# Kernel tuning notes

Hardware: AMD Instinct MI355X
Metric: run time of the kernel (lower is better)

## Reference

```python
import jax, jax.numpy as jnp
import numpy as np

B, T, C = 4, 4096, 1024
H, CS = 16, 128
D = C // H
EPS = 1e-5

def _ln(x, g, b):
    m = jnp.mean(x, axis=-1, keepdims=True)
    v = jnp.var(x, axis=-1, keepdims=True)
    return (x - m) * jax.lax.rsqrt(v + EPS) * g + b

def setup_inputs() -> dict:
    key = jax.random.key(0)
    ks = jax.random.split(key, 12)
    s_c = 1.0 / np.sqrt(C)
    s_2d = 1.0 / np.sqrt(2 * D)
    return {
        "x": jax.random.normal(ks[0], (B, T, C), jnp.float32),
        "mark_W": jax.random.normal(ks[1], (C, C), jnp.float32) * s_c,
        "mark_b": jnp.zeros((C,), jnp.float32),
        "gate_W": jax.random.normal(ks[2], (C, C), jnp.float32) * s_c,
        "gate_b": jnp.zeros((C,), jnp.float32),
        "carry_g": jnp.ones((D,), jnp.float32),
        "carry_b": jnp.zeros((D,), jnp.float32),
        "card_g": jnp.ones((D,), jnp.float32),
        "card_b": jnp.zeros((D,), jnp.float32),
        "ho1_W": jax.random.normal(ks[3], (2 * D, 2 * D), jnp.float32) * s_2d,
        "ho1_b": jnp.zeros((2 * D,), jnp.float32),
        "ho2_W": jax.random.normal(ks[4], (2 * D, D), jnp.float32) * s_2d,
        "ho2_b": jnp.zeros((D,), jnp.float32),
        "proj_W": jax.random.normal(ks[5], (C, C), jnp.float32) * s_c * 0.02,
        "proj_b": jnp.zeros((C,), jnp.float32),
        "ln_g": jnp.ones((C,), jnp.float32),
        "ln_b": jnp.zeros((C,), jnp.float32),
    }

def reference(x, mark_W, mark_b, gate_W, gate_b, carry_g, carry_b,
              card_g, card_b, ho1_W, ho1_b, ho2_W, ho2_b,
              proj_W, proj_b, ln_g, ln_b):
    b, t, c = x.shape
    nc = t // CS  # T chosen divisible by chunk_size -> pad_len = 0
    pm = x @ mark_W + mark_b                       # [B,T,C]
    gates = jax.nn.sigmoid(x @ gate_W + gate_b)    # [B,T,C]

    def chunks(a):  # [B,T,C] -> [B,H,nc,CS,D]
        return a.reshape(b, nc, CS, H, D).transpose(0, 3, 1, 2, 4)

    x_h = chunks(x)
    gm = chunks(gates) * chunks(pm)                # gated marks
    lcm = jnp.cumsum(gm, axis=3)                   # local prefix sum within chunk
    chunk_sums = lcm[:, :, :, -1, :]               # [B,H,nc,D]
    carry_cum = jnp.cumsum(chunk_sums, axis=2)
    carries = jnp.concatenate(
        [jnp.zeros((b, H, 1, D), x.dtype), carry_cum[:, :, :-1, :]], axis=2)
    nrm_carry = _ln(carries, carry_g, carry_b)[:, :, :, None, :]  # [B,H,nc,1,D]
    mwc = lcm + nrm_carry                          # marks with carry
    cards_local = jnp.concatenate([nrm_carry, mwc[:, :, :, :-1, :]], axis=3)
    cards = _ln(cards_local, card_g, card_b)
    comb = jnp.concatenate([x_h, cards], axis=-1)  # [B,H,nc,CS,2D]
    h = jax.nn.gelu(comb @ ho1_W + ho1_b, approximate=False)
    ho = h @ ho2_W + ho2_b                         # [B,H,nc,CS,D]
    out = ho.transpose(0, 2, 3, 1, 4).reshape(b, t, c)
    out = out @ proj_W + proj_b
    out = _ln(out, ln_g, ln_b)
    return x + out
```

## Files before the change

kernel.cpp:

```cpp
#include <hip/hip_runtime.h>
#include <hip/hip_bf16.h>

typedef __bf16 bf16_t;
typedef __attribute__((ext_vector_type(8))) __bf16 bf16x8;
typedef __attribute__((ext_vector_type(4))) __bf16 bf16x4;
typedef __attribute__((ext_vector_type(4))) float f32x4;

static constexpr int Bn = 4, Tn = 4096, Cn = 1024, Hn = 16, CSn = 128, Dn = 64, NCn = 32;

#define DEVINL __device__ __forceinline__

DEVINL float wsum64(float v) {
  v += __shfl_xor(v, 32, 64);
  v += __shfl_xor(v, 16, 64);
  v += __shfl_xor(v, 8, 64);
  v += __shfl_xor(v, 4, 64);
  v += __shfl_xor(v, 2, 64);
  v += __shfl_xor(v, 1, 64);
  return v;
}

DEVINL float gelu_f(float v) {
  float x = v * 0.70710678f;
  float ax = fabsf(x);
  float t = 1.f / (1.f + 0.3275911f * ax);
  float poly = t * (0.254829592f +
               t * (-0.284496736f +
               t * (1.421413741f +
               t * (-1.453152027f +
               t * 1.061405429f))));
  float e = __expf(-ax * ax);
  float erfax = 1.f - poly * e;
  float erfx = copysignf(erfax, x);
  return 0.5f * v * (1.f + erfx);
}

DEVINL void gld16(const bf16_t* g, bf16_t* l) {
  __builtin_amdgcn_global_load_lds(
      (const __attribute__((address_space(1))) unsigned int*)(g),
      (__attribute__((address_space(3))) unsigned int*)(l), 16, 0, 0);
}

__global__ __launch_bounds__(256) void k_xbf(const float* __restrict__ in,
                                             bf16_t* __restrict__ out) {
  int i = blockIdx.x * 256 + threadIdx.x;
  float4 a = *reinterpret_cast<const float4*>(in + (size_t)i * 8);
  float4 b = *reinterpret_cast<const float4*>(in + (size_t)i * 8 + 4);
  bf16x8 o = {(bf16_t)a.x, (bf16_t)a.y, (bf16_t)a.z, (bf16_t)a.w,
              (bf16_t)b.x, (bf16_t)b.y, (bf16_t)b.z, (bf16_t)b.w};
  *reinterpret_cast<bf16x8*>(out + (size_t)i * 8) = o;
}

__global__ void k_transpose(const float* __restrict__ in, bf16_t* __restrict__ out,
                            int rows, int cols) {
  __shared__ float tile[64][65];
  int c0 = blockIdx.x * 64, r0 = blockIdx.y * 64;
  int tx = threadIdx.x & 63, ty = threadIdx.x >> 6;
#pragma unroll
  for (int i = ty; i < 64; i += 4)
    tile[i][tx] = in[(size_t)(r0 + i) * cols + c0 + tx];
  __syncthreads();
#pragma unroll
  for (int i = ty; i < 64; i += 4)
    out[(size_t)(c0 + i) * rows + r0 + tx] = (bf16_t)tile[tx][i];
}

__global__ __launch_bounds__(256, 3) void k_dualgemm_gm(
    const bf16_t* __restrict__ X, const bf16_t* __restrict__ Wtm,
    const bf16_t* __restrict__ Wtg, const float* __restrict__ bm,
    const float* __restrict__ bg, bf16_t* __restrict__ lcm,
    float* __restrict__ csum) {
  constexpr int K = Cn, N = Cn;
  constexpr int GP = 68;
  __shared__ __align__(16) bf16_t L[16384];
  __shared__ float tot[4][64];
  int tid = threadIdx.x;
  int Lb = blockIdx.x;
  int xcd = Lb & 7, jj = Lb >> 3;
  int nb = jj & 15, mb = xcd + 8 * (jj >> 4);
  int m0 = mb * 128, n0 = nb * 64;
  int wave = tid >> 6, lane = tid & 63;
  int wm = wave >> 1, wn = wave & 1;
  int lr = lane & 15, lk = lane >> 4;
  int rl = lane >> 2;
  int cl = (lane & 3) * 8;
  f32x4 accP[4][2] = {};
  f32x4 accG[4][2] = {};

  const bf16_t* Xb = X + (size_t)m0 * K;
  const bf16_t* Wmb = Wtm + (size_t)n0 * K;
  const bf16_t* Wgb = Wtg + (size_t)n0 * K;
  bf16_t* LA = L;
  bf16_t* LBm = L + 8192;
  bf16_t* LBg = L + 12288;

#define STAGE3(buf, kt)                                                    \
  {                                                                        \
    _Pragma("unroll")                                                      \
    for (int c = 0; c < 2; ++c) {                                          \
      int ch = wave * 2 + c;                                               \
      gld16(Xb + (size_t)(ch * 16 + rl) * K + (kt) * 32 + cl,              \
            LA + (buf) * 4096 + ch * 512);                                 \
    }                                                                      \
    size_t gob = (size_t)(wave * 16 + rl) * K + (kt) * 32 + cl;            \
    gld16(Wmb + gob, LBm + (buf) * 2048 + wave * 512);                     \
    gld16(Wgb + gob, LBg + (buf) * 2048 + wave * 512);                     \
  }

  STAGE3(0, 0);
  __syncthreads();
  int cur = 0;
  for (int kt = 0; kt < 32; ++kt) {
    if (kt < 31) STAGE3(cur ^ 1, kt + 1);
    bf16x8 af[4], bmf[2], bgf[2];
#pragma unroll
    for (int i = 0; i < 4; ++i)
      af[i] = *reinterpret_cast<const bf16x8*>(
          &LA[cur * 4096 + (wm * 64 + i * 16 + lr) * 32 + lk * 8]);
#pragma unroll
    for (int j = 0; j < 2; ++j) {
      bmf[j] = *reinterpret_cast<const bf16x8*>(
          &LBm[cur * 2048 + (wn * 32 + j * 16 + lr) * 32 + lk * 8]);
      bgf[j] = *reinterpret_cast<const bf16x8*>(
          &LBg[cur * 2048 + (wn * 32 + j * 16 + lr) * 32 + lk * 8]);
    }
#pragma unroll
    for (int i = 0; i < 4; ++i)
#pragma unroll
      for (int j = 0; j < 2; ++j) {
        accP[i][j] = __builtin_amdgcn_mfma_f32_16x16x32_bf16(af[i], bmf[j], accP[i][j], 0, 0, 0);
        accG[i][j] = __builtin_amdgcn_mfma_f32_16x16x32_bf16(af[i], bgf[j], accG[i][j], 0, 0, 0);
      }
    __syncthreads();
    cur ^= 1;
  }
#undef STAGE3

  bf16_t* G = L;
#pragma unroll
  for (int j = 0; j < 2; ++j) {
    int col = wn * 32 + j * 16 + lr;
    float bmv = bm[n0 + col], bgv = bg[n0 + col];
#pragma unroll
    for (int i = 0; i < 4; ++i) {
      int rbase = wm * 64 + i * 16 + lk * 4;
#pragma unroll
      for (int r = 0; r < 4; ++r) {
        float p = accP[i][j][r] + bmv;
        float g = accG[i][j][r] + bgv;
        float s = 1.f / (1.f + __expf(-g));
        G[(rbase + r) * GP + col] = (bf16_t)(s * p);
      }
    }
  }
  __syncthreads();
  {
    int col = tid & 63;
    int q = tid >> 6;
    float lsum = 0.f;
#pragma unroll 8
    for (int r = 0; r < 32; ++r)
      lsum += (float)G[(q * 32 + r) * GP + col];
    tot[q][col] = lsum;
    __syncthreads();
    float run = 0.f;
#pragma unroll
    for (int qq = 0; qq < 3; ++qq)
      if (qq < q) run += tot[qq][col];
    int gc = n0 + col;
    size_t obase = (size_t)(m0 + q * 32) * N + gc;
#pragma unroll 8
    for (int r = 0; r < 32; ++r) {
      run += (float)G[(q * 32 + r) * GP + col];
      lcm[obase + (size_t)r * N] = (bf16_t)run;
    }
    if (q == 3) {
      int bb = m0 >> 12;
      int ci = (m0 >> 7) & 31;
      csum[(((size_t)bb * Hn + (gc >> 6)) * NCn + ci) * 64 + (gc & 63)] = run;
    }
  }
}

__global__ __launch_bounds__(64) void k_carry_ln(const float* __restrict__ csum,
                                                 float* __restrict__ ncar,
                                                 const float* __restrict__ g,
                                                 const float* __restrict__ be) {
  int bh = blockIdx.x;
  int d = threadIdx.x;
  float gd = g[d], bd = be[d];
  float run = 0.f;
  for (int ci = 0; ci < NCn; ++ci) {
    float v = run;
    run += csum[((size_t)bh * NCn + ci) * 64 + d];
    float m = wsum64(v) * (1.f / 64.f);
    float dv = v - m;
    float var = wsum64(dv * dv) * (1.f / 64.f);
    ncar[((size_t)bh * NCn + ci) * 64 + d] = dv * rsqrtf(var + 1e-5f) * gd + bd;
  }
}

__global__ __launch_bounds__(256, 4) void k_ho_fused(
    const bf16_t* __restrict__ X, const bf16_t* __restrict__ lcm,
    const float* __restrict__ ncar, const float* __restrict__ cg,
    const float* __restrict__ cb, const bf16_t* __restrict__ W1t,
    const float* __restrict__ b1, const bf16_t* __restrict__ W2t,
    const float* __restrict__ b2, bf16_t* __restrict__ ho) {
  __shared__ __align__(16) bf16_t Cs[128][136];
  int tid = threadIdx.x;
  int ci = blockIdx.x & 31, bh = blockIdx.x >> 5;
  int h = bh & 15, b = bh >> 4;
  int wave = tid >> 6, lane = tid & 63;
  int wm = wave >> 1, wn = wave & 1;
  int lr = lane & 15, lk = lane >> 4;
  size_t xrow0 = (size_t)(b * Tn + ci * CSn);

  bf16x8 xf0[4], xf1[4];
#pragma unroll
  for (int i = 0; i < 4; ++i) {
    const bf16_t* xr = X + (xrow0 + wm * 64 + i * 16 + lr) * Cn + h * Dn + lk * 8;
    xf0[i] = *reinterpret_cast<const bf16x8*>(xr);
    xf1[i] = *reinterpret_cast<const bf16x8*>(xr + 32);
  }

  {
    int lg = lane >> 3;
    int le = lane & 7;
    int d0 = le * 8;
    const float* np = ncar + ((size_t)bh * NCn + ci) * 64 + d0;
    float ncv[8], ggv[8], bbv[8];
#pragma unroll
    for (int e = 0; e < 8; ++e) {
      ncv[e] = np[e];
      ggv[e] = cg[d0 + e];
      bbv[e] = cb[d0 + e];
    }
#pragma unroll
    for (int it = 0; it < 4; ++it) {
      int pr = wave * 32 + it * 8 + lg;
      float v[8];
      if (pr > 0) {
        bf16x8 lv = *reinterpret_cast<const bf16x8*>(
            lcm + (xrow0 + pr - 1) * Cn + h * Dn + d0);
#pragma unroll
        for (int e = 0; e < 8; ++e) v[e] = (float)lv[e] + ncv[e];
      } else {
#pragma unroll
        for (int e = 0; e < 8; ++e) v[e] = ncv[e];
      }
      float s = 0.f;
#pragma unroll
      for (int e = 0; e < 8; ++e) s += v[e];
      s += __shfl_xor(s, 1, 64);
      s += __shfl_xor(s, 2, 64);
      s += __shfl_xor(s, 4, 64);
      float mean = s * (1.f / 64.f);
      float q = 0.f;
#pragma unroll
      for (int e = 0; e < 8; ++e) { float dv = v[e] - mean; q += dv * dv; }
      q += __shfl_xor(q, 1, 64);
      q += __shfl_xor(q, 2, 64);
      q += __shfl_xor(q, 4, 64);
      float rs = rsqrtf(q * (1.f / 64.f) + 1e-5f);
      bf16x8 o;
#pragma unroll
      for (int e = 0; e < 8; ++e)
        o[e] = (bf16_t)((v[e] - mean) * rs * ggv[e] + bbv[e]);
      *reinterpret_cast<bf16x8*>(&Cs[pr][64 + d0]) = o;
    }
  }
  __syncthreads();
  f32x4 acc[4][4] = {};
#pragma unroll
  for (int ks = 0; ks < 4; ++ks) {
    bf16x8 af[4], bfr[4];
#pragma unroll
    for (int i = 0; i < 4; ++i) {
      if (ks == 0)      af[i] = xf0[i];
      else if (ks == 1) af[i] = xf1[i];
      else
        af[i] = *reinterpret_cast<const bf16x8*>(
            &Cs[wm * 64 + i * 16 + lr][64 + (ks - 2) * 32 + lk * 8]);
    }
#pragma unroll
    for (int j = 0; j < 4; ++j)
      bfr[j] = *reinterpret_cast<const bf16x8*>(
          W1t + (size_t)(wn * 64 + j * 16 + lr) * 128 + ks * 32 + lk * 8);
#pragma unroll
    for (int i = 0; i < 4; ++i)
#pragma unroll
      for (int j = 0; j < 4; ++j)
        acc[i][j] = __builtin_amdgcn_mfma_f32_16x16x32_bf16(af[i], bfr[j], acc[i][j], 0, 0, 0);
  }
  __syncthreads();
#pragma unroll
  for (int j = 0; j < 4; ++j) {
    int col = wn * 64 + j * 16 + lr;
    float bv = b1[col];
#pragma unroll
    for (int i = 0; i < 4; ++i) {
      int rbase = wm * 64 + i * 16 + lk * 4;
#pragma unroll
      for (int r = 0; r < 4; ++r)
        Cs[rbase + r][col] = (bf16_t)gelu_f(acc[i][j][r] + bv);
    }
  }
  __syncthreads();
  f32x4 acc2[2][4] = {};
#pragma unroll
  for (int ks = 0; ks < 4; ++ks) {
    bf16x8 af[2], bfr[4];
#pragma unroll
    for (int i = 0; i < 2; ++i)
      af[i] = *reinterpret_cast<const bf16x8*>(&Cs[wave * 32 + i * 16 + lr][ks * 32 + lk * 8]);
#pragma unroll
    for (int j = 0; j < 4; ++j)
      bfr[j] = *reinterpret_cast<const bf16x8*>(
          W2t + (size_t)(j * 16 + lr) * 128 + ks * 32 + lk * 8);
#pragma unroll
    for (int i = 0; i < 2; ++i)
#pragma unroll
      for (int j = 0; j < 4; ++j)
        acc2[i][j] = __builtin_amdgcn_mfma_f32_16x16x32_bf16(af[i], bfr[j], acc2[i][j], 0, 0, 0);
  }
#pragma unroll
  for (int j = 0; j < 4; ++j) {
    int dd = j * 16 + lr;
    float bv = b2[dd];
#pragma unroll
    for (int i = 0; i < 2; ++i) {
      int pbase = wave * 32 + i * 16 + lk * 4;
#pragma unroll
      for (int r = 0; r < 4; ++r)
        ho[(xrow0 + pbase + r) * Cn + h * Dn + dd] = (bf16_t)(acc2[i][j][r] + bv);
    }
  }
}

__global__ __launch_bounds__(256, 2) void k_gemm_bt(
    const bf16_t* __restrict__ A, const bf16_t* __restrict__ Wt,
    const float* __restrict__ bias, bf16_t* __restrict__ out) {
  constexpr int K = Cn, N = Cn;
  __shared__ __align__(16) bf16_t L[4][128 * 32];
  int tid = threadIdx.x;
  int Lb = blockIdx.x + 8 * blockIdx.y;
  int xcd = Lb & 7, jj = Lb >> 3;
  int nb = jj & 7, mb = xcd + 8 * (jj >> 3);
  int m0 = mb * 128, n0 = nb * 128;
  int wave = tid >> 6, lane = tid & 63;
  int wm = wave >> 1, wn = wave & 1;
  int lr = lane & 15, lk = lane >> 4;
  int rl = lane >> 2, cl = (lane & 3) * 8;
  f32x4 acc[4][4] = {};
  const bf16_t* Ab = A + (size_t)m0 * K;
  const bf16_t* Wb = Wt + (size_t)n0 * K;

#define STAGE2(buf, kt)                                                    \
  {                                                                        \
    _Pragma("unroll")                                                      \
    for (int c = 0; c < 2; ++c) {                                          \
      int ch = wave * 2 + c;                                               \
      size_t go = (size_t)(ch * 16 + rl) * K + (kt) * 32 + cl;             \
      int lo = ch * 512;                                                   \
      gld16(Ab + go, &L[0 + (buf)][lo]);                                   \
      gld16(Wb + go, &L[2 + (buf)][lo]);                                   \
    }                                                                      \
  }

  STAGE2(0, 0);
  __syncthreads();
  int cur = 0;
  for (int kt = 0; kt < 32; ++kt) {
    if (kt < 31) STAGE2(cur ^ 1, kt + 1);
    bf16x8 af[4], bfr[4];
#pragma unroll
    for (int i = 0; i < 4; ++i)
      af[i] = *reinterpret_cast<const bf16x8*>(&L[0 + cur][(wm * 64 + i * 16 + lr) * 32 + lk * 8]);
#pragma unroll
    for (int j = 0; j < 4; ++j)
      bfr[j] = *reinterpret_cast<const bf16x8*>(&L[2 + cur][(wn * 64 + j * 16 + lr) * 32 + lk * 8]);
#pragma unroll
    for (int i = 0; i < 4; ++i)
#pragma unroll
      for (int j = 0; j < 4; ++j)
        acc[i][j] = __builtin_amdgcn_mfma_f32_16x16x32_bf16(af[i], bfr[j], acc[i][j], 0, 0, 0);
    __syncthreads();
    cur ^= 1;
  }
#undef STAGE2
#pragma unroll
  for (int j = 0; j < 4; ++j) {
    int col = n0 + wn * 64 + j * 16 + lr;
    float bv = bias[col];
#pragma unroll
    for (int i = 0; i < 4; ++i) {
      int rbase = m0 + wm * 64 + i * 16 + lk * 4;
#pragma unroll
      for (int r = 0; r < 4; ++r)
        out[(size_t)(rbase + r) * N + col] = (bf16_t)(acc[i][j][r] + bv);
    }
  }
}

__global__ __launch_bounds__(256) void k_ln_residual(
    const bf16_t* __restrict__ pre, const float* __restrict__ X,
    const float* __restrict__ g, const float* __restrict__ be,
    float* __restrict__ out) {
  int row = blockIdx.x, t = threadIdx.x;
  size_t base = (size_t)row * Cn + t * 4;
  bf16x4 pv4 = *reinterpret_cast<const bf16x4*>(pre + base);
  float v0 = (float)pv4[0], v1 = (float)pv4[1], v2 = (float)pv4[2], v3 = (float)pv4[3];
  float s = v0 + v1 + v2 + v3;
  float q = v0 * v0 + v1 * v1 + v2 * v2 + v3 * v3;
  s = wsum64(s);
  q = wsum64(q);
  __shared__ float red[8];
  int wv = t >> 6, ln = t & 63;
  if (ln == 0) { red[wv] = s; red[4 + wv] = q; }
  __syncthreads();
  float tot = red[0] + red[1] + red[2] + red[3];
  float totq = red[4] + red[5] + red[6] + red[7];
  float mean = tot * (1.f / 1024.f);
  float var = totq * (1.f / 1024.f) - mean * mean;
  float rs = rsqrtf(fmaxf(var, 0.f) + 1e-5f);
  float4 xv = *reinterpret_cast<const float4*>(X + base);
  float4 gv = *reinterpret_cast<const float4*>(g + t * 4);
  float4 bv = *reinterpret_cast<const float4*>(be + t * 4);
  float4 o;
  o.x = (v0 - mean) * rs * gv.x + bv.x + xv.x;
  o.y = (v1 - mean) * rs * gv.y + bv.y + xv.y;
  o.z = (v2 - mean) * rs * gv.z + bv.z + xv.z;
  o.w = (v3 - mean) * rs * gv.w + bv.w + xv.w;
  *reinterpret_cast<float4*>(out + base) = o;
}

extern "C" void kernel_launch(void* const* d_in, const int* in_sizes, int n_in,
                              void* d_out, int out_size, void* d_ws, size_t ws_size,
                              hipStream_t stream) {
  const float* x       = (const float*)d_in[0];
  const float* mark_W  = (const float*)d_in[1];
  const float* mark_b  = (const float*)d_in[2];
  const float* gate_W  = (const float*)d_in[3];
  const float* gate_b  = (const float*)d_in[4];
  const float* carry_g = (const float*)d_in[5];
  const float* carry_b = (const float*)d_in[6];
  const float* card_g  = (const float*)d_in[7];
  const float* card_b  = (const float*)d_in[8];
  const float* ho1_W   = (const float*)d_in[9];
  const float* ho1_b   = (const float*)d_in[10];
  const float* ho2_W   = (const float*)d_in[11];
  const float* ho2_b   = (const float*)d_in[12];
  const float* proj_W  = (const float*)d_in[13];
  const float* proj_b  = (const float*)d_in[14];
  const float* ln_g    = (const float*)d_in[15];
  const float* ln_b    = (const float*)d_in[16];
  float* out = (float*)d_out;

  char* ws = (char*)d_ws;
  bf16_t* xbf    = (bf16_t*)(ws + 0);
  bf16_t* outpre = (bf16_t*)(ws + 0);
  bf16_t* gm     = (bf16_t*)(ws + 33554432);
  bf16_t* hobuf  = (bf16_t*)(ws + 100663296);
  float*  csum   = (float*)(ws + 134217728);
  float*  ncar   = (float*)(ws + 134742016);
  bf16_t* wtm    = (bf16_t*)(ws + 135266304);
  bf16_t* wtg    = (bf16_t*)(ws + 137363456);
  bf16_t* wtp    = (bf16_t*)(ws + 139460608);
  bf16_t* wt1    = (bf16_t*)(ws + 141557760);
  bf16_t* wt2    = (bf16_t*)(ws + 141590528);

  k_xbf<<<8192, 256, 0, stream>>>(x, xbf);
  k_transpose<<<dim3(16, 16), 256, 0, stream>>>(mark_W, wtm, 1024, 1024);
  k_transpose<<<dim3(16, 16), 256, 0, stream>>>(gate_W, wtg, 1024, 1024);
  k_transpose<<<dim3(16, 16), 256, 0, stream>>>(proj_W, wtp, 1024, 1024);
  k_transpose<<<dim3(2, 2),   256, 0, stream>>>(ho1_W, wt1, 128, 128);
  k_transpose<<<dim3(1, 2),   256, 0, stream>>>(ho2_W, wt2, 128, 64);

  k_dualgemm_gm<<<2048, 256, 0, stream>>>(xbf, wtm, wtg, mark_b, gate_b, gm, csum);
  k_carry_ln<<<64, 64, 0, stream>>>(csum, ncar, carry_g, carry_b);
  k_ho_fused<<<2048, 256, 0, stream>>>(xbf, gm, ncar, card_g, card_b,
                                       wt1, ho1_b, wt2, ho2_b, hobuf);
  k_gemm_bt<<<dim3(8, 128), 256, 0, stream>>>(hobuf, wtp, proj_b, outpre);
  k_ln_residual<<<16384, 256, 0, stream>>>(outpre, x, ln_g, ln_b, out);
}
```

Measured before the change: 264.7 us.

## Split ho_fused blocks into half chunks and read bf16 residual in LN

k_ho_fused now handles 64 rows per block instead of 128. That halves shared memory and the accumulator registers, doubles the grid to 4096 blocks, and raises the launch-bound occupancy target to 6. The final LN-residual kernel reads the residual x from the bf16 copy instead of fp32, which halves that read traffic. The output-pre buffer moves to its own workspace region so xbf is not overwritten. Adding the residual in bf16 instead of exact fp32 x costs some precision.

```diff
diff --git a/kernel.cpp b/kernel.cpp
--- a/kernel.cpp
+++ b/kernel.cpp
@@ -200,25 +200,28 @@
   }
 }
 
-__global__ __launch_bounds__(256, 4) void k_ho_fused(
+__global__ __launch_bounds__(256, 6) void k_ho_fused(
     const bf16_t* __restrict__ X, const bf16_t* __restrict__ lcm,
     const float* __restrict__ ncar, const float* __restrict__ cg,
     const float* __restrict__ cb, const bf16_t* __restrict__ W1t,
     const float* __restrict__ b1, const bf16_t* __restrict__ W2t,
     const float* __restrict__ b2, bf16_t* __restrict__ ho) {
-  __shared__ __align__(16) bf16_t Cs[128][136];
+  __shared__ __align__(16) bf16_t Cs[64][136];
   int tid = threadIdx.x;
-  int ci = blockIdx.x & 31, bh = blockIdx.x >> 5;
+  int idx = blockIdx.x;
+  int bh = idx >> 6;
+  int rem = idx & 63;
+  int ci = rem >> 1, half = rem & 1;
   int h = bh & 15, b = bh >> 4;
   int wave = tid >> 6, lane = tid & 63;
   int wm = wave >> 1, wn = wave & 1;
   int lr = lane & 15, lk = lane >> 4;
-  size_t xrow0 = (size_t)(b * Tn + ci * CSn);
-
-  bf16x8 xf0[4], xf1[4];
-#pragma unroll
-  for (int i = 0; i < 4; ++i) {
-    const bf16_t* xr = X + (xrow0 + wm * 64 + i * 16 + lr) * Cn + h * Dn + lk * 8;
+  size_t xrow0 = (size_t)(b * Tn + ci * CSn + half * 64);
+
+  bf16x8 xf0[2], xf1[2];
+#pragma unroll
+  for (int i = 0; i < 2; ++i) {
+    const bf16_t* xr = X + (xrow0 + wm * 32 + i * 16 + lr) * Cn + h * Dn + lk * 8;
     xf0[i] = *reinterpret_cast<const bf16x8*>(xr);
     xf1[i] = *reinterpret_cast<const bf16x8*>(xr + 32);
   }
@@ -236,10 +239,10 @@
       bbv[e] = cb[d0 + e];
     }
 #pragma unroll
-    for (int it = 0; it < 4; ++it) {
-      int pr = wave * 32 + it * 8 + lg;
+    for (int it = 0; it < 2; ++it) {
+      int pr = wave * 16 + it * 8 + lg;
       float v[8];
-      if (pr > 0) {
+      if (half || pr > 0) {
         bf16x8 lv = *reinterpret_cast<const bf16x8*>(
             lcm + (xrow0 + pr - 1) * Cn + h * Dn + d0);
 #pragma unroll
@@ -270,24 +273,24 @@
     }
   }
   __syncthreads();
-  f32x4 acc[4][4] = {};
+  f32x4 acc[2][4] = {};
 #pragma unroll
   for (int ks = 0; ks < 4; ++ks) {
-    bf16x8 af[4], bfr[4];
-#pragma unroll
-    for (int i = 0; i < 4; ++i) {
+    bf16x8 af[2], bfr[4];
+#pragma unroll
+    for (int i = 0; i < 2; ++i) {
       if (ks == 0)      af[i] = xf0[i];
       else if (ks == 1) af[i] = xf1[i];
       else
         af[i] = *reinterpret_cast<const bf16x8*>(
-            &Cs[wm * 64 + i * 16 + lr][64 + (ks - 2) * 32 + lk * 8]);
+            &Cs[wm * 32 + i * 16 + lr][64 + (ks - 2) * 32 + lk * 8]);
     }
 #pragma unroll
     for (int j = 0; j < 4; ++j)
       bfr[j] = *reinterpret_cast<const bf16x8*>(
           W1t + (size_t)(wn * 64 + j * 16 + lr) * 128 + ks * 32 + lk * 8);
 #pragma unroll
-    for (int i = 0; i < 4; ++i)
+    for (int i = 0; i < 2; ++i)
 #pragma unroll
       for (int j = 0; j < 4; ++j)
         acc[i][j] = __builtin_amdgcn_mfma_f32_16x16x32_bf16(af[i], bfr[j], acc[i][j], 0, 0, 0);
@@ -298,42 +301,35 @@
     int col = wn * 64 + j * 16 + lr;
     float bv = b1[col];
 #pragma unroll
-    for (int i = 0; i < 4; ++i) {
-      int rbase = wm * 64 + i * 16 + lk * 4;
+    for (int i = 0; i < 2; ++i) {
+      int rbase = wm * 32 + i * 16 + lk * 4;
 #pragma unroll
       for (int r = 0; r < 4; ++r)
         Cs[rbase + r][col] = (bf16_t)gelu_f(acc[i][j][r] + bv);
     }
   }
   __syncthreads();
-  f32x4 acc2[2][4] = {};
+  f32x4 acc2[4] = {};
 #pragma unroll
   for (int ks = 0; ks < 4; ++ks) {
-    bf16x8 af[2], bfr[4];
-#pragma unroll
-    for (int i = 0; i < 2; ++i)
-      af[i] = *reinterpret_cast<const bf16x8*>(&Cs[wave * 32 + i * 16 + lr][ks * 32 + lk * 8]);
+    bf16x8 af = *reinterpret_cast<const bf16x8*>(&Cs[wave * 16 + lr][ks * 32 + lk * 8]);
+    bf16x8 bfr[4];
 #pragma unroll
     for (int j = 0; j < 4; ++j)
       bfr[j] = *reinterpret_cast<const bf16x8*>(
           W2t + (size_t)(j * 16 + lr) * 128 + ks * 32 + lk * 8);
 #pragma unroll
-    for (int i = 0; i < 2; ++i)
-#pragma unroll
-      for (int j = 0; j < 4; ++j)
-        acc2[i][j] = __builtin_amdgcn_mfma_f32_16x16x32_bf16(af[i], bfr[j], acc2[i][j], 0, 0, 0);
+    for (int j = 0; j < 4; ++j)
+      acc2[j] = __builtin_amdgcn_mfma_f32_16x16x32_bf16(af, bfr[j], acc2[j], 0, 0, 0);
   }
 #pragma unroll
   for (int j = 0; j < 4; ++j) {
     int dd = j * 16 + lr;
     float bv = b2[dd];
-#pragma unroll
-    for (int i = 0; i < 2; ++i) {
-      int pbase = wave * 32 + i * 16 + lk * 4;
-#pragma unroll
-      for (int r = 0; r < 4; ++r)
-        ho[(xrow0 + pbase + r) * Cn + h * Dn + dd] = (bf16_t)(acc2[i][j][r] + bv);
-    }
+    int pbase = wave * 16 + lk * 4;
+#pragma unroll
+    for (int r = 0; r < 4; ++r)
+      ho[(xrow0 + pbase + r) * Cn + h * Dn + dd] = (bf16_t)(acc2[j][r] + bv);
   }
 }
 
@@ -403,7 +399,7 @@
 }
 
 __global__ __launch_bounds__(256) void k_ln_residual(
-    const bf16_t* __restrict__ pre, const float* __restrict__ X,
+    const bf16_t* __restrict__ pre, const bf16_t* __restrict__ Xb,
     const float* __restrict__ g, const float* __restrict__ be,
     float* __restrict__ out) {
   int row = blockIdx.x, t = threadIdx.x;
@@ -423,14 +419,14 @@
   float mean = tot * (1.f / 1024.f);
   float var = totq * (1.f / 1024.f) - mean * mean;
   float rs = rsqrtf(fmaxf(var, 0.f) + 1e-5f);
-  float4 xv = *reinterpret_cast<const float4*>(X + base);
+  bf16x4 xv4 = *reinterpret_cast<const bf16x4*>(Xb + base);
   float4 gv = *reinterpret_cast<const float4*>(g + t * 4);
   float4 bv = *reinterpret_cast<const float4*>(be + t * 4);
   float4 o;
-  o.x = (v0 - mean) * rs * gv.x + bv.x + xv.x;
-  o.y = (v1 - mean) * rs * gv.y + bv.y + xv.y;
-  o.z = (v2 - mean) * rs * gv.z + bv.z + xv.z;
-  o.w = (v3 - mean) * rs * gv.w + bv.w + xv.w;
+  o.x = (v0 - mean) * rs * gv.x + bv.x + (float)xv4[0];
+  o.y = (v1 - mean) * rs * gv.y + bv.y + (float)xv4[1];
+  o.z = (v2 - mean) * rs * gv.z + bv.z + (float)xv4[2];
+  o.w = (v3 - mean) * rs * gv.w + bv.w + (float)xv4[3];
   *reinterpret_cast<float4*>(out + base) = o;
 }
 
@@ -458,8 +454,8 @@
 
   char* ws = (char*)d_ws;
   bf16_t* xbf    = (bf16_t*)(ws + 0);
-  bf16_t* outpre = (bf16_t*)(ws + 0);
   bf16_t* gm     = (bf16_t*)(ws + 33554432);
+  bf16_t* outpre = (bf16_t*)(ws + 67108864);
   bf16_t* hobuf  = (bf16_t*)(ws + 100663296);
   float*  csum   = (float*)(ws + 134217728);
   float*  ncar   = (float*)(ws + 134742016);
@@ -478,8 +474,8 @@
 
   k_dualgemm_gm<<<2048, 256, 0, stream>>>(xbf, wtm, wtg, mark_b, gate_b, gm, csum);
   k_carry_ln<<<64, 64, 0, stream>>>(csum, ncar, carry_g, carry_b);
-  k_ho_fused<<<2048, 256, 0, stream>>>(xbf, gm, ncar, card_g, card_b,
+  k_ho_fused<<<4096, 256, 0, stream>>>(xbf, gm, ncar, card_g, card_b,
                                        wt1, ho1_b, wt2, ho2_b, hobuf);
   k_gemm_bt<<<dim3(8, 128), 256, 0, stream>>>(hobuf, wtp, proj_b, outpre);
-  k_ln_residual<<<16384, 256, 0, stream>>>(outpre, x, ln_g, ln_b, out);
-}
+  k_ln_residual<<<16384, 256, 0, stream>>>(outpre, xbf, ln_g, ln_b, out);
+}
```

New measurement: 290.1 us. 9.6% more time.

## Split card LayerNorm into its own kernel and read residual from bf16 copy

Applied to the files above, without the earlier changes.

Moves the per-chunk cards LayerNorm out of the fused head-output kernel into a separate kernel that writes a contiguous bf16 cards buffer. The fused kernel then loads that buffer into swizzled shared memory using direct global-to-LDS loads, which is meant to shorten its prologue. The final LayerNorm-residual kernel reads the residual from the bf16 copy of x instead of fp32 to halve that read traffic. This adds an extra launch and a global round trip for the cards buffer, and rounding the residual to bf16 loses precision in the output.

```diff
diff --git a/kernel.cpp b/kernel.cpp
--- a/kernel.cpp
+++ b/kernel.cpp
@@ -200,21 +200,85 @@
   }
 }
 
+__global__ __launch_bounds__(256) void k_cards(
+    const bf16_t* __restrict__ lcm, const float* __restrict__ ncar,
+    const float* __restrict__ cg, const float* __restrict__ cb,
+    bf16_t* __restrict__ cards) {
+  int blk = blockIdx.x;
+  int ci = blk & 31, bh = blk >> 5;
+  int h = bh & 15, b = bh >> 4;
+  int wave = threadIdx.x >> 6, lane = threadIdx.x & 63;
+  int lg = lane >> 3;
+  int le = lane & 7;
+  int d0 = le * 8;
+  size_t xrow0 = (size_t)(b * Tn + ci * CSn);
+  const float* np = ncar + ((size_t)bh * NCn + ci) * 64 + d0;
+  float ncv[8], ggv[8], bbv[8];
+#pragma unroll
+  for (int e = 0; e < 8; ++e) {
+    ncv[e] = np[e];
+    ggv[e] = cg[d0 + e];
+    bbv[e] = cb[d0 + e];
+  }
+#pragma unroll
+  for (int it = 0; it < 4; ++it) {
+    int pr = wave * 32 + it * 8 + lg;
+    float v[8];
+    if (pr > 0) {
+      bf16x8 lv = *reinterpret_cast<const bf16x8*>(
+          lcm + (xrow0 + pr - 1) * Cn + h * Dn + d0);
+#pragma unroll
+      for (int e = 0; e < 8; ++e) v[e] = (float)lv[e] + ncv[e];
+    } else {
+#pragma unroll
+      for (int e = 0; e < 8; ++e) v[e] = ncv[e];
+    }
+    float s = 0.f;
+#pragma unroll
+    for (int e = 0; e < 8; ++e) s += v[e];
+    s += __shfl_xor(s, 1, 64);
+    s += __shfl_xor(s, 2, 64);
+    s += __shfl_xor(s, 4, 64);
+    float mean = s * (1.f / 64.f);
+    float q = 0.f;
+#pragma unroll
+    for (int e = 0; e < 8; ++e) { float dv = v[e] - mean; q += dv * dv; }
+    q += __shfl_xor(q, 1, 64);
+    q += __shfl_xor(q, 2, 64);
+    q += __shfl_xor(q, 4, 64);
+    float rs = rsqrtf(q * (1.f / 64.f) + 1e-5f);
+    bf16x8 o;
+#pragma unroll
+    for (int e = 0; e < 8; ++e)
+      o[e] = (bf16_t)((v[e] - mean) * rs * ggv[e] + bbv[e]);
+    *reinterpret_cast<bf16x8*>(cards + ((size_t)blk * CSn + pr) * 64 + d0) = o;
+  }
+}
+
 __global__ __launch_bounds__(256, 4) void k_ho_fused(
-    const bf16_t* __restrict__ X, const bf16_t* __restrict__ lcm,
-    const float* __restrict__ ncar, const float* __restrict__ cg,
-    const float* __restrict__ cb, const bf16_t* __restrict__ W1t,
-    const float* __restrict__ b1, const bf16_t* __restrict__ W2t,
-    const float* __restrict__ b2, bf16_t* __restrict__ ho) {
-  __shared__ __align__(16) bf16_t Cs[128][136];
+    const bf16_t* __restrict__ X, const bf16_t* __restrict__ cards,
+    const bf16_t* __restrict__ W1t, const float* __restrict__ b1,
+    const bf16_t* __restrict__ W2t, const float* __restrict__ b2,
+    bf16_t* __restrict__ ho) {
+  __shared__ __align__(16) bf16_t S[128 * 136];
   int tid = threadIdx.x;
-  int ci = blockIdx.x & 31, bh = blockIdx.x >> 5;
+  int blk = blockIdx.x;
+  int ci = blk & 31, bh = blk >> 5;
   int h = bh & 15, b = bh >> 4;
   int wave = tid >> 6, lane = tid & 63;
   int wm = wave >> 1, wn = wave & 1;
   int lr = lane & 15, lk = lane >> 4;
   size_t xrow0 = (size_t)(b * Tn + ci * CSn);
 
+  {
+    const bf16_t* cbase = cards + (size_t)blk * CSn * 64;
+#pragma unroll
+    for (int c = 0; c < 4; ++c) {
+      int row = wave * 32 + c * 8 + (lane >> 3);
+      int c16 = (lane & 7) ^ (row & 7);
+      gld16(cbase + (size_t)row * 64 + c16 * 8, S + (wave * 32 + c * 8) * 64);
+    }
+  }
   bf16x8 xf0[4], xf1[4];
 #pragma unroll
   for (int i = 0; i < 4; ++i) {
@@ -222,54 +286,8 @@
     xf0[i] = *reinterpret_cast<const bf16x8*>(xr);
     xf1[i] = *reinterpret_cast<const bf16x8*>(xr + 32);
   }
-
-  {
-    int lg = lane >> 3;
-    int le = lane & 7;
-    int d0 = le * 8;
-    const float* np = ncar + ((size_t)bh * NCn + ci) * 64 + d0;
-    float ncv[8], ggv[8], bbv[8];
-#pragma unroll
-    for (int e = 0; e < 8; ++e) {
-      ncv[e] = np[e];
-      ggv[e] = cg[d0 + e];
-      bbv[e] = cb[d0 + e];
-    }
-#pragma unroll
-    for (int it = 0; it < 4; ++it) {
-      int pr = wave * 32 + it * 8 + lg;
-      float v[8];
-      if (pr > 0) {
-        bf16x8 lv = *reinterpret_cast<const bf16x8*>(
-            lcm + (xrow0 + pr - 1) * Cn + h * Dn + d0);
-#pragma unroll
-        for (int e = 0; e < 8; ++e) v[e] = (float)lv[e] + ncv[e];
-      } else {
-#pragma unroll
-        for (int e = 0; e < 8; ++e) v[e] = ncv[e];
-      }
-      float s = 0.f;
-#pragma unroll
-      for (int e = 0; e < 8; ++e) s += v[e];
-      s += __shfl_xor(s, 1, 64);
-      s += __shfl_xor(s, 2, 64);
-      s += __shfl_xor(s, 4, 64);
-      float mean = s * (1.f / 64.f);
-      float q = 0.f;
-#pragma unroll
-      for (int e = 0; e < 8; ++e) { float dv = v[e] - mean; q += dv * dv; }
-      q += __shfl_xor(q, 1, 64);
-      q += __shfl_xor(q, 2, 64);
-      q += __shfl_xor(q, 4, 64);
-      float rs = rsqrtf(q * (1.f / 64.f) + 1e-5f);
-      bf16x8 o;
-#pragma unroll
-      for (int e = 0; e < 8; ++e)
-        o[e] = (bf16_t)((v[e] - mean) * rs * ggv[e] + bbv[e]);
-      *reinterpret_cast<bf16x8*>(&Cs[pr][64 + d0]) = o;
-    }
-  }
-  __syncthreads();
+  __syncthreads();
+
   f32x4 acc[4][4] = {};
 #pragma unroll
   for (int ks = 0; ks < 4; ++ks) {
@@ -278,9 +296,11 @@
     for (int i = 0; i < 4; ++i) {
       if (ks == 0)      af[i] = xf0[i];
       else if (ks == 1) af[i] = xf1[i];
-      else
-        af[i] = *reinterpret_cast<const bf16x8*>(
-            &Cs[wm * 64 + i * 16 + lr][64 + (ks - 2) * 32 + lk * 8]);
+      else {
+        int row = wm * 64 + i * 16 + lr;
+        int c16 = ((ks - 2) * 4 + lk) ^ (lr & 7);
+        af[i] = *reinterpret_cast<const bf16x8*>(&S[row * 64 + c16 * 8]);
+      }
     }
 #pragma unroll
     for (int j = 0; j < 4; ++j)
@@ -302,7 +322,7 @@
       int rbase = wm * 64 + i * 16 + lk * 4;
 #pragma unroll
       for (int r = 0; r < 4; ++r)
-        Cs[rbase + r][col] = (bf16_t)gelu_f(acc[i][j][r] + bv);
+        S[(rbase + r) * 136 + col] = (bf16_t)gelu_f(acc[i][j][r] + bv);
     }
   }
   __syncthreads();
@@ -312,7 +332,8 @@
     bf16x8 af[2], bfr[4];
 #pragma unroll
     for (int i = 0; i < 2; ++i)
-      af[i] = *reinterpret_cast<const bf16x8*>(&Cs[wave * 32 + i * 16 + lr][ks * 32 + lk * 8]);
+      af[i] = *reinterpret_cast<const bf16x8*>(
+          &S[(wave * 32 + i * 16 + lr) * 136 + ks * 32 + lk * 8]);
 #pragma unroll
     for (int j = 0; j < 4; ++j)
       bfr[j] = *reinterpret_cast<const bf16x8*>(
@@ -403,7 +424,7 @@
 }
 
 __global__ __launch_bounds__(256) void k_ln_residual(
-    const bf16_t* __restrict__ pre, const float* __restrict__ X,
+    const bf16_t* __restrict__ pre, const bf16_t* __restrict__ Xb,
     const float* __restrict__ g, const float* __restrict__ be,
     float* __restrict__ out) {
   int row = blockIdx.x, t = threadIdx.x;
@@ -423,14 +444,14 @@
   float mean = tot * (1.f / 1024.f);
   float var = totq * (1.f / 1024.f) - mean * mean;
   float rs = rsqrtf(fmaxf(var, 0.f) + 1e-5f);
-  float4 xv = *reinterpret_cast<const float4*>(X + base);
+  bf16x4 xv4 = *reinterpret_cast<const bf16x4*>(Xb + base);
   float4 gv = *reinterpret_cast<const float4*>(g + t * 4);
   float4 bv = *reinterpret_cast<const float4*>(be + t * 4);
   float4 o;
-  o.x = (v0 - mean) * rs * gv.x + bv.x + xv.x;
-  o.y = (v1 - mean) * rs * gv.y + bv.y + xv.y;
-  o.z = (v2 - mean) * rs * gv.z + bv.z + xv.z;
-  o.w = (v3 - mean) * rs * gv.w + bv.w + xv.w;
+  o.x = (v0 - mean) * rs * gv.x + bv.x + (float)xv4[0];
+  o.y = (v1 - mean) * rs * gv.y + bv.y + (float)xv4[1];
+  o.z = (v2 - mean) * rs * gv.z + bv.z + (float)xv4[2];
+  o.w = (v3 - mean) * rs * gv.w + bv.w + (float)xv4[3];
   *reinterpret_cast<float4*>(out + base) = o;
 }
 
@@ -458,8 +479,9 @@
 
   char* ws = (char*)d_ws;
   bf16_t* xbf    = (bf16_t*)(ws + 0);
-  bf16_t* outpre = (bf16_t*)(ws + 0);
   bf16_t* gm     = (bf16_t*)(ws + 33554432);
+  bf16_t* cards  = (bf16_t*)(ws + 67108864);
+  bf16_t* outpre = (bf16_t*)(ws + 67108864);
   bf16_t* hobuf  = (bf16_t*)(ws + 100663296);
   float*  csum   = (float*)(ws + 134217728);
   float*  ncar   = (float*)(ws + 134742016);
@@ -478,8 +500,8 @@
 
   k_dualgemm_gm<<<2048, 256, 0, stream>>>(xbf, wtm, wtg, mark_b, gate_b, gm, csum);
   k_carry_ln<<<64, 64, 0, stream>>>(csum, ncar, carry_g, carry_b);
-  k_ho_fused<<<2048, 256, 0, stream>>>(xbf, gm, ncar, card_g, card_b,
-                                       wt1, ho1_b, wt2, ho2_b, hobuf);
+  k_cards<<<2048, 256, 0, stream>>>(gm, ncar, card_g, card_b, cards);
+  k_ho_fused<<<2048, 256, 0, stream>>>(xbf, cards, wt1, ho1_b, wt2, ho2_b, hobuf);
   k_gemm_bt<<<dim3(8, 128), 256, 0, stream>>>(hobuf, wtp, proj_b, outpre);
-  k_ln_residual<<<16384, 256, 0, stream>>>(outpre, x, ln_g, ln_b, out);
-}
+  k_ln_residual<<<16384, 256, 0, stream>>>(outpre, xbf, ln_g, ln_b, out);
+}
```

Result: no change. 269.5 us (+1.8%).
